# Performance work log

Hardware: AMD Instinct MI355X
Metric: run time of the kernel (lower is better)

Reference implementation:

```python
import jax, jax.numpy as jnp
import numpy as np

B = 512; LH = 200; N = 40000; F = 256; E = 2000000; EF = 4
K = 8; LP = 50; P = 5000; D = 64; TD = 16; SK = 1000


def _time_enc(t):
    # TimeDualDecayEncoder stand-in: fixed log-spaced frequency cosine features (TGAT-style)
    freqs = 1.0 / (10.0 ** (jnp.arange(TD, dtype=jnp.float32) / TD * 5.0))
    return jnp.cos(t[..., None] * freqs)


def _layernorm(x, g, b):
    m = x.mean(-1, keepdims=True)
    v = ((x - m) ** 2).mean(-1, keepdims=True)
    return (x - m) * jax.lax.rsqrt(v + 1e-5) * g + b


def _gru(x, Wih, Whh, bih, bhh):
    # torch nn.GRU (batch_first), gate order r,z,n; returns final hidden state
    bsz, H = x.shape[0], Whh.shape[1]
    def step(h, xt):
        gi = xt @ Wih.T + bih
        gh = h @ Whh.T + bhh
        ir, iz, inn = jnp.split(gi, 3, -1)
        hr, hz, hn = jnp.split(gh, 3, -1)
        r = jax.nn.sigmoid(ir + hr)
        z = jax.nn.sigmoid(iz + hz)
        n = jnp.tanh(inn + r * hn)
        return (1.0 - z) * n + z * h, None
    h, _ = jax.lax.scan(step, jnp.zeros((bsz, H), x.dtype), jnp.swapaxes(x, 0, 1))
    return h


def _forward(src_node_ids, dst_node_ids, local_neighbor_ids, local_edge_ids, local_times,
             dst_neighbor_ids, dst_edge_ids, dst_times, retrieved_indices,
             node_raw, edge_raw, pool_nodes,
             Wfeat, bfeat, Wedge, bedge, Wtime, btime, Wstruct, bstruct, ln_g, ln_b,
             gruL_Wih, gruL_Whh, gruL_bih, gruL_bhh, gruQ_Wih, gruQ_Whh, gruQ_bih, gruQ_bhh,
             gcn_W, gcn_b, fus_W, fus_b, out_W, out_b):

    def dygkt(nids, eids, times, cur_dst, cur_skill):
        raw = node_raw[nids]                                   # (B,L,F) gather
        nf = raw @ Wfeat.T + bfeat
        ef = edge_raw[eids, 0:1] @ Wedge.T + bedge
        tf = _time_enc(times) @ Wtime.T + btime
        co = (nids == cur_dst[:, None]).astype(jnp.float32)[..., None]
        st = co @ Wstruct.T + bstruct
        sim = (raw[..., 0].astype(jnp.int32) == cur_skill[:, None]).astype(jnp.float32)[..., None]
        sk = sim @ Wstruct.T + bstruct
        return _layernorm(nf + ef + tf + st + sk, ln_g, ln_b)

    def graph_emb(demo):
        # demo: (K,LP) padded node-id sequences (0 = pad). Build dedup'd undirected
        # consecutive-pair graph, run GCNConv (self loops, sym norm), mean-pool.
        ids = demo.reshape(-1)
        M = ids.shape[0]
        valid = ids > 0
        sids = jnp.sort(jnp.where(valid, ids, N))               # invalid -> sentinel N
        uniq = (sids < N) & jnp.concatenate([jnp.ones((1,), bool), sids[1:] != sids[:-1]])
        x = node_raw[jnp.clip(sids, 0, N - 1)] @ Wfeat.T + bfeat
        h = (x @ gcn_W.T) * uniq[:, None]
        u = demo[:, :-1].reshape(-1)
        v = demo[:, 1:].reshape(-1)
        ve = (u > 0) & (v > 0)
        a = jnp.minimum(u, v); b = jnp.maximum(u, v)
        BIG = N * N                                             # fits int32 since N=40000
        skey = jnp.sort(jnp.where(ve, a * N + b, BIG))
        ew = ((skey < BIG) & jnp.concatenate([jnp.ones((1,), bool), skey[1:] != skey[:-1]])).astype(x.dtype)
        su = jnp.clip(jnp.searchsorted(sids, skey // N), 0, M - 1)
        sv = jnp.clip(jnp.searchsorted(sids, skey % N), 0, M - 1)
        uf = uniq.astype(x.dtype)
        deg = jnp.zeros(M, x.dtype).at[su].add(ew).at[sv].add(ew) + uf   # + self loop
        dis = jnp.where(deg > 0, jax.lax.rsqrt(deg), 0.0)
        nrm = (ew * dis[su] * dis[sv])[:, None]
        agg = jnp.zeros_like(h).at[sv].add(nrm * h[su]).at[su].add(nrm * h[sv])
        agg = agg + h * (dis * dis)[:, None] + gcn_b * uf[:, None]
        out = jax.nn.relu(agg)
        return out.sum(0) / jnp.maximum(uniq.sum(), 1).astype(x.dtype)

    dst_skill = node_raw[dst_node_ids, 0].astype(jnp.int32)
    src_skill = node_raw[src_node_ids, 0].astype(jnp.int32)
    local_emb = _gru(dygkt(local_neighbor_ids, local_edge_ids, local_times, dst_node_ids, dst_skill),
                     gruL_Wih, gruL_Whh, gruL_bih, gruL_bhh)
    glob = jax.vmap(graph_emb)(pool_nodes[retrieved_indices])   # (B,D)
    q_emb = _gru(dygkt(dst_neighbor_ids, dst_edge_ids, dst_times, src_node_ids, src_skill),
                 gruQ_Wih, gruQ_Whh, gruQ_bih, gruQ_bhh)
    fused = jax.nn.relu(jnp.concatenate([local_emb, glob], 1) @ fus_W.T + fus_b)
    return fused @ out_W.T + out_b, q_emb @ out_W.T + out_b


def setup_inputs() -> dict:
    key = jax.random.key(0)
    ks = jax.random.split(key, 32)
    f32 = jnp.float32
    node_raw = jax.random.normal(ks[0], (N, F), f32)
    node_raw = node_raw.at[:, 0].set(jax.random.randint(ks[1], (N,), 0, SK).astype(f32))
    edge_raw = jax.random.normal(ks[2], (E, EF), f32)
    ids = jax.random.randint(ks[3], (P, LP), 1, N)
    lens = jax.random.randint(ks[4], (P,), 2, LP + 1)
    pool_nodes = jnp.where(jnp.arange(LP)[None, :] < lens[:, None], ids, 0).astype(jnp.int32)
    def lin(k, o, i, s=0.05):
        kw, kb = jax.random.split(k)
        return jax.random.normal(kw, (o, i), f32) * s, jax.random.normal(kb, (o,), f32) * s
    Wfeat, bfeat = lin(ks[5], D, F)
    Wedge, bedge = lin(ks[6], D, 1)
    Wtime, btime = lin(ks[7], D, TD)
    Wstruct, bstruct = lin(ks[8], D, 1)
    gruL_Wih, gruL_bih = lin(ks[9], 3 * D, D)
    gruL_Whh, gruL_bhh = lin(ks[10], 3 * D, D)
    gruQ_Wih, gruQ_bih = lin(ks[11], 3 * D, D)
    gruQ_Whh, gruQ_bhh = lin(ks[12], 3 * D, D)
    gcn_W, gcn_b = lin(ks[13], D, D)
    fus_W, fus_b = lin(ks[14], D, 2 * D)
    out_W, out_b = lin(ks[15], D, D)
    return dict(
        src_node_ids=jax.random.randint(ks[16], (B,), 0, N).astype(jnp.int32),
        dst_node_ids=jax.random.randint(ks[17], (B,), 0, N).astype(jnp.int32),
        local_neighbor_ids=jax.random.randint(ks[18], (B, LH), 0, N).astype(jnp.int32),
        local_edge_ids=jax.random.randint(ks[19], (B, LH), 0, E).astype(jnp.int32),
        local_times=jax.random.uniform(ks[20], (B, LH), f32) * 100.0,
        dst_neighbor_ids=jax.random.randint(ks[21], (B, LH), 0, N).astype(jnp.int32),
        dst_edge_ids=jax.random.randint(ks[22], (B, LH), 0, E).astype(jnp.int32),
        dst_times=jax.random.uniform(ks[23], (B, LH), f32) * 100.0,
        retrieved_indices=jax.random.randint(ks[24], (B, K), 0, P).astype(jnp.int32),
        node_raw=node_raw, edge_raw=edge_raw, pool_nodes=pool_nodes,
        Wfeat=Wfeat, bfeat=bfeat, Wedge=Wedge, bedge=bedge, Wtime=Wtime, btime=btime,
        Wstruct=Wstruct, bstruct=bstruct, ln_g=jnp.ones((D,), f32), ln_b=jnp.zeros((D,), f32),
        gruL_Wih=gruL_Wih, gruL_Whh=gruL_Whh, gruL_bih=gruL_bih, gruL_bhh=gruL_bhh,
        gruQ_Wih=gruQ_Wih, gruQ_Whh=gruQ_Whh, gruQ_bih=gruQ_bih, gruQ_bhh=gruQ_bhh,
        gcn_W=gcn_W, gcn_b=gcn_b, fus_W=fus_W, fus_b=fus_b, out_W=out_W, out_b=out_b)


def reference(src_node_ids, dst_node_ids, local_neighbor_ids, local_edge_ids, local_times,
              dst_neighbor_ids, dst_edge_ids, dst_times, retrieved_indices,
              node_raw, edge_raw, pool_nodes,
              Wfeat, bfeat, Wedge, bedge, Wtime, btime, Wstruct, bstruct, ln_g, ln_b,
              gruL_Wih, gruL_Whh, gruL_bih, gruL_bhh, gruQ_Wih, gruQ_Whh, gruQ_bih, gruQ_bhh,
              gcn_W, gcn_b, fus_W, fus_b, out_W, out_b):
    return _forward(src_node_ids, dst_node_ids, local_neighbor_ids, local_edge_ids, local_times,
                    dst_neighbor_ids, dst_edge_ids, dst_times, retrieved_indices,
                    node_raw, edge_raw, pool_nodes,
                    Wfeat, bfeat, Wedge, bedge, Wtime, btime, Wstruct, bstruct, ln_g, ln_b,
                    gruL_Wih, gruL_Whh, gruL_bih, gruL_bhh, gruQ_Wih, gruQ_Whh, gruQ_bih, gruQ_bhh,
                    gcn_W, gcn_b, fus_W, fus_b, out_W, out_b)
```

## Files before the change

kernel.cpp:

```cpp
#include <hip/hip_runtime.h>
#include <math.h>

#define NN 40000
#define FF 256
#define DD 64
#define LHH 200
#define BB 512
#define TDD 16
#define EE 2000000
#define GE_HASH 1024

typedef _Float16 h2f __attribute__((ext_vector_type(2)));

__constant__ float TFREQ[16] = {
    1.0f,            0.48696753f,    0.23713737f,    0.115478195f,
    0.056234132f,    0.027384196f,   0.013335215f,   0.0064938162f,
    0.0031622776f,   0.0015399265f,  0.00074989421f, 0.00036517414f,
    0.00017782794f,  8.6596433e-05f, 4.2169650e-05f, 2.0535251e-05f
};

__device__ __forceinline__ float fd2(unsigned a, unsigned b, float c) {
    union { unsigned u; h2f h; } ua, ub;
    ua.u = a; ub.u = b;
    return __builtin_amdgcn_fdot2(ua.h, ub.h, c, false);
}
__device__ __forceinline__ unsigned packrn(float a, float b) {
    union { h2f h; unsigned u; } x;
    x.h.x = (_Float16)a; x.h.y = (_Float16)b;
    return x.u;
}
__device__ __forceinline__ unsigned short f16u(float a) {
    union { _Float16 h; unsigned short u; } x;
    x.h = (_Float16)a;
    return x.u;
}
__device__ __forceinline__ float h16f(unsigned short u) {
    union { unsigned short u; _Float16 h; } x;
    x.u = u;
    return (float)x.h;
}
__device__ __forceinline__ float f16lo(unsigned u) {
    union { unsigned u; h2f h; } x; x.u = u; return (float)x.h.x;
}
__device__ __forceinline__ float f16hi(unsigned u) {
    union { unsigned u; h2f h; } x; x.u = u; return (float)x.h.y;
}
__device__ __forceinline__ unsigned pkrtz_u(float a, float b) {
    auto pk = __builtin_amdgcn_cvt_pkrtz(a, b);
    union { decltype(pk) h; unsigned u; } x;
    x.h = pk;
    return x.u;
}
__device__ __forceinline__ float dpp_xor1(float v) {
    return __int_as_float(
        __builtin_amdgcn_mov_dpp(__float_as_int(v), 0xB1, 0xF, 0xF, true));
}
__device__ __forceinline__ unsigned rlu(unsigned v, int l) {
    return (unsigned)__builtin_amdgcn_readlane((int)v, l);
}
__device__ __forceinline__ float sigm(float x) {
    return __builtin_amdgcn_rcpf(1.f + __expf(-x));
}
__device__ __forceinline__ float tanh_f(float x) {
    float e = __expf(2.f * x);
    return 1.f - 2.f * __builtin_amdgcn_rcpf(e + 1.f);
}
__device__ __forceinline__ int hlookupf(const unsigned* hkey, const int* hslot, unsigned id)
{
    unsigned p = (id * 2654435761u) & (GE_HASH - 1);
    while (hkey[p] != id) p = (p + 1) & (GE_HASH - 1);
    return hslot[p];
}

__global__ void __launch_bounds__(256)
compact_kernel(const float* __restrict__ node_raw, const float* __restrict__ edge_raw,
               unsigned short* __restrict__ skill16, unsigned short* __restrict__ e016)
{
    const int stride = gridDim.x * 256;
    int i = blockIdx.x * 256 + threadIdx.x;
    for (int n = i; n < NN; n += stride)
        skill16[n] = (unsigned short)(int)node_raw[(size_t)n * FF];
    for (int e = i; e < EE; e += stride)
        e016[e] = f16u(edge_raw[(size_t)e * 4]);
}

template<int KDIM>
__global__ void __launch_bounds__(256)
gemm_nt_kernel(const float* __restrict__ A, const float* __restrict__ W,
               const float* __restrict__ bias, float* __restrict__ C, int Nrows)
{
    __shared__ __align__(16) float a_t[128][8];
    __shared__ __align__(16) float wt[8][64];
    const int tid = threadIdx.x;
    const int tx = tid & 15;
    const int ty = tid >> 4;
    const int n0 = blockIdx.x * 128;

    float4 acc[8];
#pragma unroll
    for (int r = 0; r < 8; ++r) acc[r] = make_float4(0.f, 0.f, 0.f, 0.f);

    for (int kc = 0; kc < KDIM; kc += 8) {
        __syncthreads();
        {
            int r = tid >> 1;
            int cc = (tid & 1) * 4;
            int n = n0 + r;
            float4 v = make_float4(0.f, 0.f, 0.f, 0.f);
            if (n < Nrows) v = *(const float4*)(A + (size_t)n * KDIM + kc + cc);
            *(float4*)&a_t[r][cc] = v;
        }
        {
            int m = tid >> 2;
            int f0 = (tid & 3) * 2;
            float2 v = *(const float2*)(W + (size_t)m * KDIM + kc + f0);
            wt[f0][m] = v.x; wt[f0 + 1][m] = v.y;
        }
        __syncthreads();
        float4 w4[8];
#pragma unroll
        for (int f = 0; f < 8; ++f) w4[f] = *(float4*)&wt[f][tx * 4];
#pragma unroll
        for (int rr = 0; rr < 8; ++rr) {
            int row = ty + rr * 16;
            float4 a0 = *(float4*)&a_t[row][0];
            float4 a1 = *(float4*)&a_t[row][4];
            float av[8] = {a0.x, a0.y, a0.z, a0.w, a1.x, a1.y, a1.z, a1.w};
#pragma unroll
            for (int f = 0; f < 8; ++f) {
                acc[rr].x += av[f] * w4[f].x;
                acc[rr].y += av[f] * w4[f].y;
                acc[rr].z += av[f] * w4[f].z;
                acc[rr].w += av[f] * w4[f].w;
            }
        }
    }
    float4 bv = make_float4(0.f, 0.f, 0.f, 0.f);
    if (bias) bv = *(const float4*)(bias + tx * 4);
#pragma unroll
    for (int rr = 0; rr < 8; ++rr) {
        int n = n0 + ty + rr * 16;
        if (n < Nrows) {
            float4 o = acc[rr];
            o.x += bv.x; o.y += bv.y; o.z += bv.z; o.w += bv.w;
            *(float4*)(C + (size_t)n * DD + tx * 4) = o;
        }
    }
}

__global__ void __launch_bounds__(256)
tn_gemm_kernel(const float* __restrict__ proj,
               const float* __restrict__ WihL, const float* __restrict__ WihQ,
               const float* __restrict__ ln_g,
               unsigned short* __restrict__ TnL, unsigned short* __restrict__ TnQ,
               unsigned short* __restrict__ proj16)
{
    const float* Wih = blockIdx.y ? WihQ : WihL;
    unsigned short* Tn = blockIdx.y ? TnQ : TnL;
    __shared__ float wgT[64][193];
    __shared__ __align__(16) float4 at4[64][16];
    const int tid = threadIdx.x;
    const int n0 = blockIdx.x * 64;
    for (int i = tid; i < 192 * 64; i += 256) {
        int j = i >> 6, k = i & 63;
        wgT[k][j] = Wih[i] * ln_g[k];
    }
    for (int i = tid; i < 1024; i += 256) {
        int r = i >> 4, kc = i & 15;
        at4[r][kc] = ((const float4*)(proj + (size_t)(n0 + r) * DD))[kc];
    }
    __syncthreads();
    if (blockIdx.y == 0) {
        const float* atf = (const float*)at4;
        for (int i = tid; i < 64 * 64; i += 256)
            proj16[(size_t)(n0 + (i >> 6)) * DD + (i & 63)] = f16u(atf[i]);
    }
    const int c = tid & 63, wv = tid >> 6;
    float acc0[16], acc1[16], acc2[16];
#pragma unroll
    for (int r = 0; r < 16; ++r) { acc0[r] = 0.f; acc1[r] = 0.f; acc2[r] = 0.f; }
    for (int kc = 0; kc < 16; ++kc) {
        float w0[4], w1[4], w2[4];
#pragma unroll
        for (int q = 0; q < 4; ++q) {
            w0[q] = wgT[kc * 4 + q][c];
            w1[q] = wgT[kc * 4 + q][64 + c];
            w2[q] = wgT[kc * 4 + q][128 + c];
        }
#pragma unroll
        for (int r = 0; r < 16; ++r) {
            float4 a = at4[wv * 16 + r][kc];
            acc0[r] += a.x * w0[0] + a.y * w0[1] + a.z * w0[2] + a.w * w0[3];
            acc1[r] += a.x * w1[0] + a.y * w1[1] + a.z * w1[2] + a.w * w1[3];
            acc2[r] += a.x * w2[0] + a.y * w2[1] + a.z * w2[2] + a.w * w2[3];
        }
    }
#pragma unroll
    for (int r = 0; r < 16; ++r) {
        size_t row = (size_t)(n0 + wv * 16 + r) * 192;
        Tn[row + c]       = f16u(acc0[r]);
        Tn[row + 64 + c]  = f16u(acc1[r]);
        Tn[row + 128 + c] = f16u(acc2[r]);
    }
}

__global__ void __launch_bounds__(192)
consts_kernel(const float* __restrict__ WihL, const float* __restrict__ bihL,
              const float* __restrict__ WhhL, float* __restrict__ outL,
              unsigned* __restrict__ whpL, unsigned* __restrict__ tpkL,
              const float* __restrict__ WihQ, const float* __restrict__ bihQ,
              const float* __restrict__ WhhQ, float* __restrict__ outQ,
              unsigned* __restrict__ whpQ, unsigned* __restrict__ tpkQ,
              unsigned* __restrict__ wtpk,
              const float* __restrict__ ln_g, const float* __restrict__ ln_b,
              const float* __restrict__ Wedge, const float* __restrict__ bedge,
              const float* __restrict__ Wtime, const float* __restrict__ btime,
              const float* __restrict__ Wstruct, const float* __restrict__ bstruct)
{
    const float* Wih = blockIdx.x ? WihQ : WihL;
    const float* bih = blockIdx.x ? bihQ : bihL;
    const float* Whh = blockIdx.x ? WhhQ : WhhL;
    float* out = blockIdx.x ? outQ : outL;
    unsigned* whp = blockIdx.x ? whpQ : whpL;
    unsigned* tpk = blockIdx.x ? tpkQ : tpkL;
    const int j = threadIdx.x;
    float te = 0.f, tw = 0.f, t1 = 0.f, tb0 = 0.f, cc = 0.f;
    float tt[16];
#pragma unroll
    for (int t = 0; t < 16; ++t) tt[t] = 0.f;
    for (int k = 0; k < DD; ++k) {
        float wv = Wih[j * DD + k];
        float wg = wv * ln_g[k];
        te  += wg * Wedge[k];
        tw  += wg * Wstruct[k];
        t1  += wg;
        tb0 += wg * (bedge[k] + btime[k] + 2.f * bstruct[k]);
        cc  += wv * ln_b[k];
#pragma unroll
        for (int t = 0; t < 16; ++t) tt[t] += wg * Wtime[k * TDD + t];
    }
    out[0 * 192 + j] = te;
    out[1 * 192 + j] = tw;
    out[2 * 192 + j] = t1;
    out[3 * 192 + j] = tb0;
    out[4 * 192 + j] = cc + bih[j];
    for (int t = 0; t < 16; ++t) out[(5 + t) * 192 + j] = tt[t];
    for (int q = 0; q < 8; ++q)
        tpk[j * 8 + q] = packrn(tt[2 * q], tt[2 * q + 1]);
    if (blockIdx.x == 0 && j < 64)
        for (int q = 0; q < 8; ++q)
            wtpk[j * 8 + q] = packrn(Wtime[j * TDD + 2 * q], Wtime[j * TDD + 2 * q + 1]);
    for (int k2 = 0; k2 < 32; ++k2)
        whp[j * 32 + k2] = packrn(Whh[j * DD + 2 * k2], Whh[j * DD + 2 * k2 + 1]);
}

struct PS {
    int nid, skI;
    float tn0, tn1, tn2, pv, e0, t;
};

__global__ void __launch_bounds__(256)
pre_kernel(const int* __restrict__ nidsL, const int* __restrict__ eidsL,
           const float* __restrict__ timesL, const int* __restrict__ curL,
           const int* __restrict__ nidsQ, const int* __restrict__ eidsQ,
           const float* __restrict__ timesQ, const int* __restrict__ curQ,
           const unsigned short* __restrict__ skill16, const unsigned short* __restrict__ e016,
           const unsigned short* __restrict__ proj16,
           const unsigned short* __restrict__ TnL, const unsigned short* __restrict__ TnQ,
           const float* __restrict__ cstL, const float* __restrict__ cstQ,
           const unsigned* __restrict__ tpkL, const unsigned* __restrict__ tpkQ,
           const unsigned* __restrict__ wtpk,
           const float* __restrict__ bhhL, const float* __restrict__ bhhQ,
           const float* __restrict__ Wedge, const float* __restrict__ bedge,
           const float* __restrict__ Wtime, const float* __restrict__ btime,
           const float* __restrict__ Wstruct, const float* __restrict__ bstruct,
           unsigned* __restrict__ g01out, unsigned short* __restrict__ g2out)
{
    const int tid = threadIdx.x;
    const int d = tid & 63;
    const int seg = blockIdx.x * 4 + (tid >> 6);
    const int blk = seg >> 3, qq = seg & 7;
    const int g = blk >> 9, s = blk & 511;

    const int*            nids  = g ? nidsQ : nidsL;
    const int*            eids  = g ? eidsQ : eidsL;
    const float*          times = g ? timesQ : timesL;
    const int*            curp  = g ? curQ : curL;
    const unsigned short* Tn    = g ? TnQ : TnL;
    const float*          cst   = g ? cstQ : cstL;
    const unsigned*       tpk   = g ? tpkQ : tpkL;
    const float*          bhh   = g ? bhhQ : bhhL;

    unsigned tp0[8], tp1[8], tp2[8], wtp[8];
#pragma unroll
    for (int q4 = 0; q4 < 2; ++q4) {
        uint4 a = *(const uint4*)(tpk + (size_t)(0 * 64 + d) * 8 + 4 * q4);
        tp0[4*q4] = a.x; tp0[4*q4+1] = a.y; tp0[4*q4+2] = a.z; tp0[4*q4+3] = a.w;
        uint4 b = *(const uint4*)(tpk + (size_t)(1 * 64 + d) * 8 + 4 * q4);
        tp1[4*q4] = b.x; tp1[4*q4+1] = b.y; tp1[4*q4+2] = b.z; tp1[4*q4+3] = b.w;
        uint4 c = *(const uint4*)(tpk + (size_t)(2 * 64 + d) * 8 + 4 * q4);
        tp2[4*q4] = c.x; tp2[4*q4+1] = c.y; tp2[4*q4+2] = c.z; tp2[4*q4+3] = c.w;
        uint4 e = *(const uint4*)(wtpk + (size_t)d * 8 + 4 * q4);
        wtp[4*q4] = e.x; wtp[4*q4+1] = e.y; wtp[4*q4+2] = e.z; wtp[4*q4+3] = e.w;
    }
    const float TE0 = cst[0*192 + d], TE1 = cst[0*192 + 64 + d], TE2 = cst[0*192 + 128 + d];
    const float TW0 = cst[1*192 + d], TW1 = cst[1*192 + 64 + d], TW2 = cst[1*192 + 128 + d];
    const float T10 = cst[2*192 + d], T11 = cst[2*192 + 64 + d], T12 = cst[2*192 + 128 + d];
    const float TB0 = cst[3*192 + d], TB1 = cst[3*192 + 64 + d], TB2 = cst[3*192 + 128 + d];
    const float CC0 = cst[4*192 + d] + bhh[d];
    const float CC1 = cst[4*192 + 64 + d] + bhh[64 + d];
    const float CC2 = cst[4*192 + 128 + d];
    const float we_l = Wedge[d];
    const float ws_l = Wstruct[d];
    const float b0_l = bedge[d] + btime[d] + 2.f * bstruct[d];
    const float tfl  = TFREQ[d & 15];

    const int cur = curp[s];
    const int csk = (int)skill16[cur];
    const int* nrow = nids + s * LHH;
    const int* erow = eids + s * LHH;
    const float* trow = times + s * LHH;
    const int lbase = qq * 25;

    auto GATH = [&](PS& P, int i) {
        int l = lbase + i;
        int nid = nrow[l];
        int eid = erow[l];
        P.nid = nid;
        const unsigned short* tb = Tn + (size_t)nid * 192;
        P.tn0 = h16f(tb[d]);
        P.tn1 = h16f(tb[64 + d]);
        P.tn2 = h16f(tb[128 + d]);
        P.pv  = h16f(proj16[(size_t)nid * DD + d]);
        P.e0  = h16f(e016[eid]);
        P.skI = (int)skill16[nid];
        P.t   = trow[l];
    };

    auto EMIT = [&](const PS& P, int i) {
        float cv = __cosf(P.t * tfl);
        float cx = dpp_xor1(cv);
        unsigned cp = pkrtz_u(cv, cx);
        unsigned s0 = rlu(cp, 0),  s1 = rlu(cp, 2),  s2 = rlu(cp, 4),  s3 = rlu(cp, 6);
        unsigned s4 = rlu(cp, 8),  s5 = rlu(cp, 10), s6 = rlu(cp, 12), s7 = rlu(cp, 14);
        float tf = fd2(wtp[7], s7, fd2(wtp[6], s6, fd2(wtp[5], s5, fd2(wtp[4], s4, 0.f))));
        tf = fd2(wtp[3], s3, fd2(wtp[2], s2, fd2(wtp[1], s1, fd2(wtp[0], s0, tf))));
        float flg = ((P.nid == cur) ? 1.f : 0.f) + ((P.skI == csk) ? 1.f : 0.f);
        float f = P.pv + P.e0 * we_l + flg * ws_l + b0_l + tf;
        float mu = f;
#pragma unroll
        for (int off = 32; off; off >>= 1) mu += __shfl_xor(mu, off);
        mu *= (1.f / 64.f);
        float dv = f - mu, var = dv * dv;
#pragma unroll
        for (int off = 32; off; off >>= 1) var += __shfl_xor(var, off);
        float rs = rsqrtf(var * (1.f / 64.f) + 1e-5f);
        float c0 = fd2(tp0[7], s7, fd2(tp0[6], s6, fd2(tp0[5], s5, fd2(tp0[4], s4, 0.f))));
        c0 = fd2(tp0[3], s3, fd2(tp0[2], s2, fd2(tp0[1], s1, fd2(tp0[0], s0, c0))));
        float c1 = fd2(tp1[7], s7, fd2(tp1[6], s6, fd2(tp1[5], s5, fd2(tp1[4], s4, 0.f))));
        c1 = fd2(tp1[3], s3, fd2(tp1[2], s2, fd2(tp1[1], s1, fd2(tp1[0], s0, c1))));
        float c2 = fd2(tp2[7], s7, fd2(tp2[6], s6, fd2(tp2[5], s5, fd2(tp2[4], s4, 0.f))));
        c2 = fd2(tp2[3], s3, fd2(tp2[2], s2, fd2(tp2[1], s1, fd2(tp2[0], s0, c2))));
        float g0 = (c0 + P.tn0 + P.e0 * TE0 + flg * TW0 + TB0 - mu * T10) * rs + CC0;
        float g1 = (c1 + P.tn1 + P.e0 * TE1 + flg * TW1 + TB1 - mu * T11) * rs + CC1;
        float g2 = (c2 + P.tn2 + P.e0 * TE2 + flg * TW2 + TB2 - mu * T12) * rs + CC2;
        size_t pos = ((size_t)blk * LHH + (lbase + i)) * 64 + d;
        g01out[pos] = packrn(g0, g1);
        g2out[pos] = f16u(g2);
    };

    PS A, B, C;
    GATH(A, 0);
    GATH(B, 1);
    for (int i = 0; i < 25; ++i) {
        int inext = (i + 2 < 25) ? i + 2 : 24;
        GATH(C, inext);
        EMIT(A, i);
        A = B; B = C;
    }
}

__global__ void __launch_bounds__(64) __attribute__((amdgpu_waves_per_eu(1, 1)))
gru_lite_kernel(const unsigned* __restrict__ g01, const unsigned short* __restrict__ g2a,
                const unsigned* __restrict__ whpL, const unsigned* __restrict__ whpQ,
                const float* __restrict__ bhhL, const float* __restrict__ bhhQ,
                float* __restrict__ embL, float* __restrict__ embQ)
{
    const int blk = blockIdx.x;
    const int g = blk >> 9, s = blk & 511;
    const int d = threadIdx.x;

    const unsigned* whp = g ? whpQ : whpL;
    const float*    bhh = g ? bhhQ : bhhL;
    float*          emb = g ? embQ : embL;

    unsigned w0[32], w1[32], w2[32];
    {
        const unsigned* p0 = whp + (size_t)d * 32;
        const unsigned* p1 = whp + (size_t)(64 + d) * 32;
        const unsigned* p2 = whp + (size_t)(128 + d) * 32;
#pragma unroll
        for (int q4 = 0; q4 < 8; ++q4) {
            uint4 a = *(const uint4*)(p0 + 4 * q4);
            w0[4*q4] = a.x; w0[4*q4+1] = a.y; w0[4*q4+2] = a.z; w0[4*q4+3] = a.w;
            uint4 b = *(const uint4*)(p1 + 4 * q4);
            w1[4*q4] = b.x; w1[4*q4+1] = b.y; w1[4*q4+2] = b.z; w1[4*q4+3] = b.w;
            uint4 c = *(const uint4*)(p2 + 4 * q4);
            w2[4*q4] = c.x; w2[4*q4+1] = c.y; w2[4*q4+2] = c.z; w2[4*q4+3] = c.w;
        }
    }
#pragma unroll
    for (int i = 0; i < 32; ++i) {
        asm volatile("" : "+v"(w0[i]));
        asm volatile("" : "+v"(w1[i]));
        asm volatile("" : "+v"(w2[i]));
    }
    const float BH2 = bhh[128 + d];

    const unsigned* p01 = g01 + (size_t)blk * LHH * 64 + d;
    const unsigned short* p2 = g2a + (size_t)blk * LHH * 64 + d;

    float h = 0.f;

    auto COMPUTE = [&](unsigned pk01, unsigned pk2) {
        float g0 = f16lo(pk01), g1 = f16hi(pk01);
        float g2 = h16f((unsigned short)pk2);
        float hx = dpp_xor1(h);
        unsigned hpu = pkrtz_u(h, hx);
        float a0 = 0.f, a1 = 0.f, a2 = 0.f, e0 = 0.f, e1 = 0.f, e2 = 0.f;
#pragma unroll
        for (int q = 0; q < 32; q += 2) {
            unsigned sa = rlu(hpu, 2 * q);
            unsigned sb = rlu(hpu, 2 * q + 2);
            a0 = fd2(w0[q], sa, a0);
            a1 = fd2(w1[q], sa, a1);
            a2 = fd2(w2[q], sa, a2);
            e0 = fd2(w0[q+1], sb, e0);
            e1 = fd2(w1[q+1], sb, e1);
            e2 = fd2(w2[q+1], sb, e2);
        }
        float mv0 = a0 + e0, mv1 = a1 + e1, mv2 = a2 + e2;
        float r = sigm(g0 + mv0);
        float z = sigm(g1 + mv1);
        float n = tanh_f(g2 + r * (mv2 + BH2));
        h = (1.f - z) * n + z * h;
    };

    unsigned A01[4], A2[4], B01[4], B2[4];
#pragma unroll
    for (int i = 0; i < 4; ++i) {
        A01[i] = p01[(size_t)i * 64];
        A2[i]  = p2[(size_t)i * 64];
    }
    for (int l = 0; l < LHH; l += 8) {
#pragma unroll
        for (int i = 0; i < 4; ++i) {
            int ll = l + 4 + i;
            B01[i] = p01[(size_t)ll * 64];
            B2[i]  = p2[(size_t)ll * 64];
        }
#pragma unroll
        for (int i = 0; i < 4; ++i) COMPUTE(A01[i], A2[i]);
#pragma unroll
        for (int i = 0; i < 4; ++i) {
            int ll = l + 8 + i;
            if (ll > LHH - 1) ll = LHH - 1;
            A01[i] = p01[(size_t)ll * 64];
            A2[i]  = p2[(size_t)ll * 64];
        }
#pragma unroll
        for (int i = 0; i < 4; ++i) COMPUTE(B01[i], B2[i]);
    }
    emb[(size_t)s * DD + d] = h;
}

__global__ void __launch_bounds__(512)
dedup_kernel(const int* __restrict__ retrieved, const int* __restrict__ pool_nodes,
             int* __restrict__ slot_idG, float* __restrict__ disG,
             unsigned* __restrict__ startG, unsigned short* __restrict__ adjG,
             int* __restrict__ Ub)
{
    __shared__ unsigned hkey[GE_HASH];
    __shared__ int hslot[GE_HASH];
    __shared__ unsigned ekey[GE_HASH];
    __shared__ int ids[400];
    __shared__ int slot_id[400];
    __shared__ unsigned deg[400];
    __shared__ float dis[400];
    __shared__ unsigned elist[400];
    __shared__ unsigned scanA[400], scanB[400];
    __shared__ int cursor[400];
    __shared__ unsigned short adjS[800];
    __shared__ int pids[8];
    __shared__ int cntU, cntE;

    const int b = blockIdx.x;
    const int tid = threadIdx.x;

    if (tid < 8) pids[tid] = retrieved[b * 8 + tid];
    if (tid == 0) { cntU = 0; cntE = 0; }
    for (int i = tid; i < GE_HASH; i += 512) { hkey[i] = 0u; ekey[i] = 0u; }
    if (tid < 400) deg[tid] = 0u;
    __syncthreads();

    if (tid < 400) {
        int k = tid / 50, p = tid % 50;
        ids[tid] = pool_nodes[(size_t)pids[k] * 50 + p];
    }
    __syncthreads();

    if (tid < 400) {
        int idi = ids[tid];
        if (idi > 0) {
            unsigned id = (unsigned)idi;
            unsigned p = (id * 2654435761u) & (GE_HASH - 1);
            while (true) {
                unsigned old = atomicCAS(&hkey[p], 0u, id);
                if (old == 0u) {
                    int s = atomicAdd(&cntU, 1);
                    hslot[p] = s; slot_id[s] = idi;
                    break;
                }
                if (old == id) break;
                p = (p + 1) & (GE_HASH - 1);
            }
        }
    }
    __syncthreads();

    if (tid < 8 * 49) {
        int k = tid / 49, p = tid % 49;
        int u = ids[k * 50 + p], v = ids[k * 50 + p + 1];
        if (u > 0 && v > 0) {
            unsigned a = (unsigned)min(u, v), bb = (unsigned)max(u, v);
            unsigned key = a * 40000u + bb;
            unsigned p2 = (key * 2654435761u) & (GE_HASH - 1);
            while (true) {
                unsigned old = atomicCAS(&ekey[p2], 0u, key);
                if (old == 0u) {
                    int su = hlookupf(hkey, hslot, a);
                    int sv = hlookupf(hkey, hslot, bb);
                    int e = atomicAdd(&cntE, 1);
                    elist[e] = ((unsigned)su << 16) | (unsigned)sv;
                    atomicAdd(&deg[su], 1u);
                    atomicAdd(&deg[sv], 1u);
                    break;
                }
                if (old == key) break;
                p2 = (p2 + 1) & (GE_HASH - 1);
            }
        }
    }
    __syncthreads();

    const int U = cntU, EC = cntE;
    if (tid < 400) {
        dis[tid] = rsqrtf((float)deg[tid] + 1.0f);
        scanA[tid] = deg[tid];
    }
    __syncthreads();

    unsigned* src = scanA;
    unsigned* dst = scanB;
    for (int off = 1; off < 400; off <<= 1) {
        if (tid < 400)
            dst[tid] = src[tid] + ((tid >= off) ? src[tid - off] : 0u);
        __syncthreads();
        unsigned* t = src; src = dst; dst = t;
    }
    if (tid < 400) {
        unsigned st = src[tid] - deg[tid];
        cursor[tid] = (int)st;
        if (tid < U) startG[(size_t)b * 404 + tid] = st;
    }
    if (tid == 0) {
        startG[(size_t)b * 404 + U] = (U > 0) ? src[U - 1] : 0u;
        Ub[b] = U;
    }
    __syncthreads();

    if (tid < EC) {
        unsigned pk = elist[tid];
        int su = (int)(pk >> 16), sv = (int)(pk & 0xffffu);
        int pu = atomicAdd(&cursor[su], 1);
        adjS[pu] = (unsigned short)sv;
        int pv = atomicAdd(&cursor[sv], 1);
        adjS[pv] = (unsigned short)su;
    }
    __syncthreads();

    if (tid < 400) {
        slot_idG[(size_t)b * 400 + tid] = (tid < U) ? slot_id[tid] : 0;
        disG[(size_t)b * 400 + tid] = dis[tid];
    }
    for (int i = tid; i < 800; i += 512) {
        unsigned tot = (U > 0) ? src[U - 1] : 0u;
        adjG[(size_t)b * 800 + i] = (i < (int)tot) ? adjS[i] : (unsigned short)0;
    }
}

__global__ void __launch_bounds__(256)
gcn_agg_kernel(const float* __restrict__ hgcn, const float* __restrict__ gcn_b,
               const int* __restrict__ slot_idG, const float* __restrict__ disG,
               const unsigned* __restrict__ startG, const unsigned short* __restrict__ adjG,
               const int* __restrict__ Ub, float* __restrict__ part)
{
    __shared__ int sidS[400];
    __shared__ float disS[400];
    __shared__ unsigned stS[404];
    __shared__ unsigned short adjS[800];
    __shared__ float red[4][64];

    const int b = blockIdx.x, q = blockIdx.y;
    const int tid = threadIdx.x;
    const int lane = tid & 63, w = tid >> 6;
    const int U = Ub[b];

    for (int i = tid; i < 400; i += 256) {
        sidS[i] = slot_idG[(size_t)b * 400 + i];
        disS[i] = disG[(size_t)b * 400 + i];
    }
    for (int i = tid; i < 404; i += 256) stS[i] = startG[(size_t)b * 404 + i];
    for (int i = tid; i < 800; i += 256) adjS[i] = adjG[(size_t)b * 800 + i];
    __syncthreads();

    const float gb = gcn_b[lane];
    float acc = 0.f;

    for (int s = q * 4 + w; s < U; s += 16) {
        int nid = sidS[s];
        float ds = disS[s];
        float v = fmaf(ds * ds, hgcn[(size_t)nid * 64 + lane], gb);
        int a0 = (int)stS[s];
        int cnt = (int)stS[s + 1] - a0;
        for (int e0 = 0; e0 < cnt; e0 += 4) {
            float hv[4], nr[4];
#pragma unroll
            for (int j = 0; j < 4; ++j) {
                int e = e0 + j;
                int ec = (e < cnt) ? e : cnt - 1;
                int o = adjS[a0 + ec];
                nr[j] = (e < cnt) ? ds * disS[o] : 0.f;
                hv[j] = hgcn[(size_t)sidS[o] * 64 + lane];
            }
            v += nr[0] * hv[0] + nr[1] * hv[1] + nr[2] * hv[2] + nr[3] * hv[3];
        }
        acc += fmaxf(v, 0.f);
    }

    red[w][lane] = acc;
    __syncthreads();
    if (tid < 64)
        part[((size_t)b * 4 + q) * 64 + tid] =
            red[0][tid] + red[1][tid] + red[2][tid] + red[3][tid];
}

__global__ void __launch_bounds__(64)
head_kernel(const float* __restrict__ local_emb, const float* __restrict__ part,
            const int* __restrict__ Ub, const float* __restrict__ q_emb,
            const float* __restrict__ fus_W, const float* __restrict__ fus_b,
            const float* __restrict__ out_W, const float* __restrict__ out_b,
            float* __restrict__ out)
{
    __shared__ float cat[128];
    __shared__ float fus[64];
    __shared__ float qv[64];
    const int b = blockIdx.x, d = threadIdx.x;
    cat[d] = local_emb[(size_t)b * 64 + d];
    {
        const float* pb = part + (size_t)b * 4 * 64;
        float gsum = pb[d] + pb[64 + d] + pb[128 + d] + pb[192 + d];
        cat[64 + d] = gsum / (float)max(Ub[b], 1);
    }
    qv[d] = q_emb[(size_t)b * 64 + d];
    __syncthreads();
    float acc = fus_b[d];
    const float* fw = fus_W + (size_t)d * 128;
#pragma unroll 4
    for (int k = 0; k < 128; ++k) acc += cat[k] * fw[k];
    fus[d] = fmaxf(acc, 0.f);
    __syncthreads();
    float o0 = out_b[d], o1 = out_b[d];
    const float* ow = out_W + (size_t)d * 64;
#pragma unroll 4
    for (int k = 0; k < 64; ++k) { float ww = ow[k]; o0 += fus[k] * ww; o1 += qv[k] * ww; }
    out[(size_t)b * 64 + d] = o0;
    out[(size_t)BB * 64 + (size_t)b * 64 + d] = o1;
}

extern "C" void kernel_launch(void* const* d_in, const int* in_sizes, int n_in,
                              void* d_out, int out_size, void* d_ws, size_t ws_size,
                              hipStream_t stream)
{
    const int*   src_ids    = (const int*)d_in[0];
    const int*   dst_ids    = (const int*)d_in[1];
    const int*   l_nids     = (const int*)d_in[2];
    const int*   l_eids     = (const int*)d_in[3];
    const float* l_times    = (const float*)d_in[4];
    const int*   d_nids     = (const int*)d_in[5];
    const int*   d_eids     = (const int*)d_in[6];
    const float* d_times    = (const float*)d_in[7];
    const int*   retr       = (const int*)d_in[8];
    const float* node_raw   = (const float*)d_in[9];
    const float* edge_raw   = (const float*)d_in[10];
    const int*   pool_nodes = (const int*)d_in[11];
    const float* Wfeat  = (const float*)d_in[12];
    const float* bfeat  = (const float*)d_in[13];
    const float* Wedge  = (const float*)d_in[14];
    const float* bedge  = (const float*)d_in[15];
    const float* Wtime  = (const float*)d_in[16];
    const float* btime  = (const float*)d_in[17];
    const float* Wstruct= (const float*)d_in[18];
    const float* bstruct= (const float*)d_in[19];
    const float* ln_g   = (const float*)d_in[20];
    const float* ln_b   = (const float*)d_in[21];
    const float* gruL_Wih = (const float*)d_in[22];
    const float* gruL_Whh = (const float*)d_in[23];
    const float* gruL_bih = (const float*)d_in[24];
    const float* gruL_bhh = (const float*)d_in[25];
    const float* gruQ_Wih = (const float*)d_in[26];
    const float* gruQ_Whh = (const float*)d_in[27];
    const float* gruQ_bih = (const float*)d_in[28];
    const float* gruQ_bhh = (const float*)d_in[29];
    const float* gcn_W  = (const float*)d_in[30];
    const float* gcn_b  = (const float*)d_in[31];
    const float* fus_W  = (const float*)d_in[32];
    const float* fus_b  = (const float*)d_in[33];
    const float* out_W  = (const float*)d_in[34];
    const float* out_b  = (const float*)d_in[35];

    char* wsb = (char*)d_ws;
    auto alloc = [&](size_t bytes) -> void* {
        void* p = (void*)wsb;
        wsb += (bytes + 255) & ~(size_t)255;
        return p;
    };
    float*          proj_node = (float*)alloc((size_t)NN * DD * 4);
    float*          hgcn      = (float*)alloc((size_t)NN * DD * 4);
    unsigned short* TnL16     = (unsigned short*)alloc((size_t)NN * 192 * 2);
    unsigned short* TnQ16     = (unsigned short*)alloc((size_t)NN * 192 * 2);
    unsigned short* proj16    = (unsigned short*)alloc((size_t)NN * DD * 2);
    unsigned short* skill16   = (unsigned short*)alloc((size_t)NN * 2);
    unsigned short* e016      = (unsigned short*)alloc((size_t)EE * 2);
    float*          cstL      = (float*)alloc(4096 * 4);
    float*          cstQ      = (float*)alloc(4096 * 4);
    unsigned*       whpL      = (unsigned*)alloc(192 * 32 * 4);
    unsigned*       whpQ      = (unsigned*)alloc(192 * 32 * 4);
    unsigned*       tpkL      = (unsigned*)alloc(192 * 8 * 4);
    unsigned*       tpkQ      = (unsigned*)alloc(192 * 8 * 4);
    unsigned*       wtpk      = (unsigned*)alloc(64 * 8 * 4);
    unsigned*       g01       = (unsigned*)alloc((size_t)2 * BB * LHH * 64 * 4);
    unsigned short* g2a       = (unsigned short*)alloc((size_t)2 * BB * LHH * 64 * 2);
    int*            slot_idG  = (int*)alloc((size_t)BB * 400 * 4);
    float*          disG      = (float*)alloc((size_t)BB * 400 * 4);
    unsigned*       startG    = (unsigned*)alloc((size_t)BB * 404 * 4);
    unsigned short* adjG      = (unsigned short*)alloc((size_t)BB * 800 * 2);
    int*            Ubuf      = (int*)alloc((size_t)BB * 4);
    float*          part      = (float*)alloc((size_t)BB * 4 * 64 * 4);
    float*          local_emb = (float*)alloc((size_t)BB * DD * 4);
    float*          q_emb     = (float*)alloc((size_t)BB * DD * 4);

    dim3 g1((NN + 127) / 128);
    gemm_nt_kernel<FF><<<g1, 256, 0, stream>>>(node_raw, Wfeat, bfeat, proj_node, NN);

    compact_kernel<<<2048, 256, 0, stream>>>(node_raw, edge_raw, skill16, e016);

    consts_kernel<<<2, 192, 0, stream>>>(gruL_Wih, gruL_bih, gruL_Whh, cstL, whpL, tpkL,
                                         gruQ_Wih, gruQ_bih, gruQ_Whh, cstQ, whpQ, tpkQ,
                                         wtpk, ln_g, ln_b, Wedge, bedge, Wtime, btime,
                                         Wstruct, bstruct);

    tn_gemm_kernel<<<dim3(NN / 64, 2), 256, 0, stream>>>(proj_node, gruL_Wih, gruQ_Wih,
                                                         ln_g, TnL16, TnQ16, proj16);

    dedup_kernel<<<BB, 512, 0, stream>>>(retr, pool_nodes, slot_idG, disG,
                                         startG, adjG, Ubuf);

    pre_kernel<<<2 * BB * 2, 256, 0, stream>>>(
        l_nids, l_eids, l_times, dst_ids,
        d_nids, d_eids, d_times, src_ids,
        skill16, e016, proj16, TnL16, TnQ16, cstL, cstQ,
        tpkL, tpkQ, wtpk, gruL_bhh, gruQ_bhh,
        Wedge, bedge, Wtime, btime, Wstruct, bstruct,
        g01, g2a);

    gemm_nt_kernel<DD><<<g1, 256, 0, stream>>>(proj_node, gcn_W, nullptr, hgcn, NN);

    gru_lite_kernel<<<2 * BB, 64, 0, stream>>>(
        g01, g2a, whpL, whpQ, gruL_bhh, gruQ_bhh, local_emb, q_emb);

    gcn_agg_kernel<<<dim3(BB, 4), 256, 0, stream>>>(
        hgcn, gcn_b, slot_idG, disG, startG, adjG, Ubuf, part);

    head_kernel<<<BB, 64, 0, stream>>>(local_emb, part, Ubuf, q_emb,
        fus_W, fus_b, out_W, out_b, (float*)d_out);
}
```

Baseline: 302.9 us.

## Fuse GRU and GCN aggregation into one tail kernel; drop edge compaction pass

Removes the compact pass that converted all 2M edge features to fp16; pre_kernel now reads edge_raw directly for only the gathered edges. Merges gru_lite and gcn_agg into a single tail kernel where the first blocks run GRU recurrences (4 sequences per 256-thread block) and the rest do GCN aggregation, so the latency-bound GRU overlaps the aggregation work. The hgcn GEMM is moved earlier in the launch order. This trades lower GRU occupancy and a branchy kernel for fewer launches and much less edge-compaction traffic.

```diff
diff --git a/kernel.cpp b/kernel.cpp
--- a/kernel.cpp
+++ b/kernel.cpp
@@ -73,15 +73,10 @@
 }
 
 __global__ void __launch_bounds__(256)
-compact_kernel(const float* __restrict__ node_raw, const float* __restrict__ edge_raw,
-               unsigned short* __restrict__ skill16, unsigned short* __restrict__ e016)
-{
-    const int stride = gridDim.x * 256;
+compact_kernel(const float* __restrict__ node_raw, unsigned short* __restrict__ skill16)
+{
     int i = blockIdx.x * 256 + threadIdx.x;
-    for (int n = i; n < NN; n += stride)
-        skill16[n] = (unsigned short)(int)node_raw[(size_t)n * FF];
-    for (int e = i; e < EE; e += stride)
-        e016[e] = f16u(edge_raw[(size_t)e * 4]);
+    if (i < NN) skill16[i] = (unsigned short)(int)node_raw[(size_t)i * FF];
 }
 
 template<int KDIM>
@@ -264,7 +259,7 @@
            const float* __restrict__ timesL, const int* __restrict__ curL,
            const int* __restrict__ nidsQ, const int* __restrict__ eidsQ,
            const float* __restrict__ timesQ, const int* __restrict__ curQ,
-           const unsigned short* __restrict__ skill16, const unsigned short* __restrict__ e016,
+           const unsigned short* __restrict__ skill16, const float* __restrict__ edge_raw,
            const unsigned short* __restrict__ proj16,
            const unsigned short* __restrict__ TnL, const unsigned short* __restrict__ TnQ,
            const float* __restrict__ cstL, const float* __restrict__ cstQ,
@@ -332,7 +327,7 @@
         P.tn1 = h16f(tb[64 + d]);
         P.tn2 = h16f(tb[128 + d]);
         P.pv  = h16f(proj16[(size_t)nid * DD + d]);
-        P.e0  = h16f(e016[eid]);
+        P.e0  = edge_raw[(size_t)eid * 4];
         P.skI = (int)skill16[nid];
         P.t   = trow[l];
     };
@@ -378,100 +373,6 @@
         EMIT(A, i);
         A = B; B = C;
     }
-}
-
-__global__ void __launch_bounds__(64) __attribute__((amdgpu_waves_per_eu(1, 1)))
-gru_lite_kernel(const unsigned* __restrict__ g01, const unsigned short* __restrict__ g2a,
-                const unsigned* __restrict__ whpL, const unsigned* __restrict__ whpQ,
-                const float* __restrict__ bhhL, const float* __restrict__ bhhQ,
-                float* __restrict__ embL, float* __restrict__ embQ)
-{
-    const int blk = blockIdx.x;
-    const int g = blk >> 9, s = blk & 511;
-    const int d = threadIdx.x;
-
-    const unsigned* whp = g ? whpQ : whpL;
-    const float*    bhh = g ? bhhQ : bhhL;
-    float*          emb = g ? embQ : embL;
-
-    unsigned w0[32], w1[32], w2[32];
-    {
-        const unsigned* p0 = whp + (size_t)d * 32;
-        const unsigned* p1 = whp + (size_t)(64 + d) * 32;
-        const unsigned* p2 = whp + (size_t)(128 + d) * 32;
-#pragma unroll
-        for (int q4 = 0; q4 < 8; ++q4) {
-            uint4 a = *(const uint4*)(p0 + 4 * q4);
-            w0[4*q4] = a.x; w0[4*q4+1] = a.y; w0[4*q4+2] = a.z; w0[4*q4+3] = a.w;
-            uint4 b = *(const uint4*)(p1 + 4 * q4);
-            w1[4*q4] = b.x; w1[4*q4+1] = b.y; w1[4*q4+2] = b.z; w1[4*q4+3] = b.w;
-            uint4 c = *(const uint4*)(p2 + 4 * q4);
-            w2[4*q4] = c.x; w2[4*q4+1] = c.y; w2[4*q4+2] = c.z; w2[4*q4+3] = c.w;
-        }
-    }
-#pragma unroll
-    for (int i = 0; i < 32; ++i) {
-        asm volatile("" : "+v"(w0[i]));
-        asm volatile("" : "+v"(w1[i]));
-        asm volatile("" : "+v"(w2[i]));
-    }
-    const float BH2 = bhh[128 + d];
-
-    const unsigned* p01 = g01 + (size_t)blk * LHH * 64 + d;
-    const unsigned short* p2 = g2a + (size_t)blk * LHH * 64 + d;
-
-    float h = 0.f;
-
-    auto COMPUTE = [&](unsigned pk01, unsigned pk2) {
-        float g0 = f16lo(pk01), g1 = f16hi(pk01);
-        float g2 = h16f((unsigned short)pk2);
-        float hx = dpp_xor1(h);
-        unsigned hpu = pkrtz_u(h, hx);
-        float a0 = 0.f, a1 = 0.f, a2 = 0.f, e0 = 0.f, e1 = 0.f, e2 = 0.f;
-#pragma unroll
-        for (int q = 0; q < 32; q += 2) {
-            unsigned sa = rlu(hpu, 2 * q);
-            unsigned sb = rlu(hpu, 2 * q + 2);
-            a0 = fd2(w0[q], sa, a0);
-            a1 = fd2(w1[q], sa, a1);
-            a2 = fd2(w2[q], sa, a2);
-            e0 = fd2(w0[q+1], sb, e0);
-            e1 = fd2(w1[q+1], sb, e1);
-            e2 = fd2(w2[q+1], sb, e2);
-        }
-        float mv0 = a0 + e0, mv1 = a1 + e1, mv2 = a2 + e2;
-        float r = sigm(g0 + mv0);
-        float z = sigm(g1 + mv1);
-        float n = tanh_f(g2 + r * (mv2 + BH2));
-        h = (1.f - z) * n + z * h;
-    };
-
-    unsigned A01[4], A2[4], B01[4], B2[4];
-#pragma unroll
-    for (int i = 0; i < 4; ++i) {
-        A01[i] = p01[(size_t)i * 64];
-        A2[i]  = p2[(size_t)i * 64];
-    }
-    for (int l = 0; l < LHH; l += 8) {
-#pragma unroll
-        for (int i = 0; i < 4; ++i) {
-            int ll = l + 4 + i;
-            B01[i] = p01[(size_t)ll * 64];
-            B2[i]  = p2[(size_t)ll * 64];
-        }
-#pragma unroll
-        for (int i = 0; i < 4; ++i) COMPUTE(A01[i], A2[i]);
-#pragma unroll
-        for (int i = 0; i < 4; ++i) {
-            int ll = l + 8 + i;
-            if (ll > LHH - 1) ll = LHH - 1;
-            A01[i] = p01[(size_t)ll * 64];
-            A2[i]  = p2[(size_t)ll * 64];
-        }
-#pragma unroll
-        for (int i = 0; i < 4; ++i) COMPUTE(B01[i], B2[i]);
-    }
-    emb[(size_t)s * DD + d] = h;
 }
 
 __global__ void __launch_bounds__(512)
@@ -599,11 +500,17 @@
     }
 }
 
-__global__ void __launch_bounds__(256)
-gcn_agg_kernel(const float* __restrict__ hgcn, const float* __restrict__ gcn_b,
-               const int* __restrict__ slot_idG, const float* __restrict__ disG,
-               const unsigned* __restrict__ startG, const unsigned short* __restrict__ adjG,
-               const int* __restrict__ Ub, float* __restrict__ part)
+#define GRU_BLKS 256
+
+__global__ void __launch_bounds__(256) __attribute__((amdgpu_waves_per_eu(1, 2)))
+tail_kernel(const unsigned* __restrict__ g01, const unsigned short* __restrict__ g2a,
+            const unsigned* __restrict__ whpL, const unsigned* __restrict__ whpQ,
+            const float* __restrict__ bhhL, const float* __restrict__ bhhQ,
+            float* __restrict__ embL, float* __restrict__ embQ,
+            const float* __restrict__ hgcn, const float* __restrict__ gcn_b,
+            const int* __restrict__ slot_idG, const float* __restrict__ disG,
+            const unsigned* __restrict__ startG, const unsigned short* __restrict__ adjG,
+            const int* __restrict__ Ub, float* __restrict__ part)
 {
     __shared__ int sidS[400];
     __shared__ float disS[400];
@@ -611,48 +518,139 @@
     __shared__ unsigned short adjS[800];
     __shared__ float red[4][64];
 
-    const int b = blockIdx.x, q = blockIdx.y;
     const int tid = threadIdx.x;
-    const int lane = tid & 63, w = tid >> 6;
-    const int U = Ub[b];
-
-    for (int i = tid; i < 400; i += 256) {
-        sidS[i] = slot_idG[(size_t)b * 400 + i];
-        disS[i] = disG[(size_t)b * 400 + i];
-    }
-    for (int i = tid; i < 404; i += 256) stS[i] = startG[(size_t)b * 404 + i];
-    for (int i = tid; i < 800; i += 256) adjS[i] = adjG[(size_t)b * 800 + i];
-    __syncthreads();
-
-    const float gb = gcn_b[lane];
-    float acc = 0.f;
-
-    for (int s = q * 4 + w; s < U; s += 16) {
-        int nid = sidS[s];
-        float ds = disS[s];
-        float v = fmaf(ds * ds, hgcn[(size_t)nid * 64 + lane], gb);
-        int a0 = (int)stS[s];
-        int cnt = (int)stS[s + 1] - a0;
-        for (int e0 = 0; e0 < cnt; e0 += 4) {
-            float hv[4], nr[4];
-#pragma unroll
-            for (int j = 0; j < 4; ++j) {
-                int e = e0 + j;
-                int ec = (e < cnt) ? e : cnt - 1;
-                int o = adjS[a0 + ec];
-                nr[j] = (e < cnt) ? ds * disS[o] : 0.f;
-                hv[j] = hgcn[(size_t)sidS[o] * 64 + lane];
+
+    if (blockIdx.x < GRU_BLKS) {
+        const int blk = blockIdx.x * 4 + (tid >> 6);
+        const int g = blk >> 9, s = blk & 511;
+        const int d = tid & 63;
+
+        const unsigned* whp = g ? whpQ : whpL;
+        const float*    bhh = g ? bhhQ : bhhL;
+        float*          emb = g ? embQ : embL;
+
+        unsigned w0[32], w1[32], w2[32];
+        {
+            const unsigned* p0 = whp + (size_t)d * 32;
+            const unsigned* p1 = whp + (size_t)(64 + d) * 32;
+            const unsigned* p2 = whp + (size_t)(128 + d) * 32;
+#pragma unroll
+            for (int q4 = 0; q4 < 8; ++q4) {
+                uint4 a = *(const uint4*)(p0 + 4 * q4);
+                w0[4*q4] = a.x; w0[4*q4+1] = a.y; w0[4*q4+2] = a.z; w0[4*q4+3] = a.w;
+                uint4 b = *(const uint4*)(p1 + 4 * q4);
+                w1[4*q4] = b.x; w1[4*q4+1] = b.y; w1[4*q4+2] = b.z; w1[4*q4+3] = b.w;
+                uint4 c = *(const uint4*)(p2 + 4 * q4);
+                w2[4*q4] = c.x; w2[4*q4+1] = c.y; w2[4*q4+2] = c.z; w2[4*q4+3] = c.w;
             }
-            v += nr[0] * hv[0] + nr[1] * hv[1] + nr[2] * hv[2] + nr[3] * hv[3];
-        }
-        acc += fmaxf(v, 0.f);
-    }
-
-    red[w][lane] = acc;
-    __syncthreads();
-    if (tid < 64)
-        part[((size_t)b * 4 + q) * 64 + tid] =
-            red[0][tid] + red[1][tid] + red[2][tid] + red[3][tid];
+        }
+#pragma unroll
+        for (int i = 0; i < 32; ++i) {
+            asm volatile("" : "+v"(w0[i]));
+            asm volatile("" : "+v"(w1[i]));
+            asm volatile("" : "+v"(w2[i]));
+        }
+        const float BH2 = bhh[128 + d];
+
+        const unsigned* p01 = g01 + (size_t)blk * LHH * 64 + d;
+        const unsigned short* p2 = g2a + (size_t)blk * LHH * 64 + d;
+
+        float h = 0.f;
+
+        auto COMPUTE = [&](unsigned pk01, unsigned pk2) {
+            float g0 = f16lo(pk01), g1 = f16hi(pk01);
+            float g2 = h16f((unsigned short)pk2);
+            float hx = dpp_xor1(h);
+            unsigned hpu = pkrtz_u(h, hx);
+            float a0 = 0.f, a1 = 0.f, a2 = 0.f, e0 = 0.f, e1 = 0.f, e2 = 0.f;
+#pragma unroll
+            for (int q = 0; q < 32; q += 2) {
+                unsigned sa = rlu(hpu, 2 * q);
+                unsigned sb = rlu(hpu, 2 * q + 2);
+                a0 = fd2(w0[q], sa, a0);
+                a1 = fd2(w1[q], sa, a1);
+                a2 = fd2(w2[q], sa, a2);
+                e0 = fd2(w0[q+1], sb, e0);
+                e1 = fd2(w1[q+1], sb, e1);
+                e2 = fd2(w2[q+1], sb, e2);
+            }
+            float mv0 = a0 + e0, mv1 = a1 + e1, mv2 = a2 + e2;
+            float r = sigm(g0 + mv0);
+            float z = sigm(g1 + mv1);
+            float n = tanh_f(g2 + r * (mv2 + BH2));
+            h = (1.f - z) * n + z * h;
+        };
+
+        unsigned A01[4], A2[4], B01[4], B2[4];
+#pragma unroll
+        for (int i = 0; i < 4; ++i) {
+            A01[i] = p01[(size_t)i * 64];
+            A2[i]  = p2[(size_t)i * 64];
+        }
+        for (int l = 0; l < LHH; l += 8) {
+#pragma unroll
+            for (int i = 0; i < 4; ++i) {
+                int ll = l + 4 + i;
+                B01[i] = p01[(size_t)ll * 64];
+                B2[i]  = p2[(size_t)ll * 64];
+            }
+#pragma unroll
+            for (int i = 0; i < 4; ++i) COMPUTE(A01[i], A2[i]);
+#pragma unroll
+            for (int i = 0; i < 4; ++i) {
+                int ll = l + 8 + i;
+                if (ll > LHH - 1) ll = LHH - 1;
+                A01[i] = p01[(size_t)ll * 64];
+                A2[i]  = p2[(size_t)ll * 64];
+            }
+#pragma unroll
+            for (int i = 0; i < 4; ++i) COMPUTE(B01[i], B2[i]);
+        }
+        emb[(size_t)s * DD + d] = h;
+    } else {
+        const int blk2 = blockIdx.x - GRU_BLKS;
+        const int b = blk2 >> 2, q = blk2 & 3;
+        const int lane = tid & 63, w = tid >> 6;
+        const int U = Ub[b];
+
+        for (int i = tid; i < 400; i += 256) {
+            sidS[i] = slot_idG[(size_t)b * 400 + i];
+            disS[i] = disG[(size_t)b * 400 + i];
+        }
+        for (int i = tid; i < 404; i += 256) stS[i] = startG[(size_t)b * 404 + i];
+        for (int i = tid; i < 800; i += 256) adjS[i] = adjG[(size_t)b * 800 + i];
+        __syncthreads();
+
+        const float gb = gcn_b[lane];
+        float acc = 0.f;
+
+        for (int s = q * 4 + w; s < U; s += 16) {
+            int nid = sidS[s];
+            float ds = disS[s];
+            float v = fmaf(ds * ds, hgcn[(size_t)nid * 64 + lane], gb);
+            int a0 = (int)stS[s];
+            int cnt = (int)stS[s + 1] - a0;
+            for (int e0 = 0; e0 < cnt; e0 += 4) {
+                float hv[4], nr[4];
+#pragma unroll
+                for (int j = 0; j < 4; ++j) {
+                    int e = e0 + j;
+                    int ec = (e < cnt) ? e : cnt - 1;
+                    int o = adjS[a0 + ec];
+                    nr[j] = (e < cnt) ? ds * disS[o] : 0.f;
+                    hv[j] = hgcn[(size_t)sidS[o] * 64 + lane];
+                }
+                v += nr[0] * hv[0] + nr[1] * hv[1] + nr[2] * hv[2] + nr[3] * hv[3];
+            }
+            acc += fmaxf(v, 0.f);
+        }
+
+        red[w][lane] = acc;
+        __syncthreads();
+        if (tid < 64)
+            part[((size_t)b * 4 + q) * 64 + tid] =
+                red[0][tid] + red[1][tid] + red[2][tid] + red[3][tid];
+    }
 }
 
 __global__ void __launch_bounds__(64)
@@ -741,7 +739,6 @@
     unsigned short* TnQ16     = (unsigned short*)alloc((size_t)NN * 192 * 2);
     unsigned short* proj16    = (unsigned short*)alloc((size_t)NN * DD * 2);
     unsigned short* skill16   = (unsigned short*)alloc((size_t)NN * 2);
-    unsigned short* e016      = (unsigned short*)alloc((size_t)EE * 2);
     float*          cstL      = (float*)alloc(4096 * 4);
     float*          cstQ      = (float*)alloc(4096 * 4);
     unsigned*       whpL      = (unsigned*)alloc(192 * 32 * 4);
@@ -763,13 +760,15 @@
     dim3 g1((NN + 127) / 128);
     gemm_nt_kernel<FF><<<g1, 256, 0, stream>>>(node_raw, Wfeat, bfeat, proj_node, NN);
 
-    compact_kernel<<<2048, 256, 0, stream>>>(node_raw, edge_raw, skill16, e016);
+    compact_kernel<<<(NN + 255) / 256, 256, 0, stream>>>(node_raw, skill16);
 
     consts_kernel<<<2, 192, 0, stream>>>(gruL_Wih, gruL_bih, gruL_Whh, cstL, whpL, tpkL,
                                          gruQ_Wih, gruQ_bih, gruQ_Whh, cstQ, whpQ, tpkQ,
                                          wtpk, ln_g, ln_b, Wedge, bedge, Wtime, btime,
                                          Wstruct, bstruct);
 
+    gemm_nt_kernel<DD><<<g1, 256, 0, stream>>>(proj_node, gcn_W, nullptr, hgcn, NN);
+
     tn_gemm_kernel<<<dim3(NN / 64, 2), 256, 0, stream>>>(proj_node, gruL_Wih, gruQ_Wih,
                                                          ln_g, TnL16, TnQ16, proj16);
 
@@ -779,17 +778,13 @@
     pre_kernel<<<2 * BB * 2, 256, 0, stream>>>(
         l_nids, l_eids, l_times, dst_ids,
         d_nids, d_eids, d_times, src_ids,
-        skill16, e016, proj16, TnL16, TnQ16, cstL, cstQ,
+        skill16, edge_raw, proj16, TnL16, TnQ16, cstL, cstQ,
         tpkL, tpkQ, wtpk, gruL_bhh, gruQ_bhh,
         Wedge, bedge, Wtime, btime, Wstruct, bstruct,
         g01, g2a);
 
-    gemm_nt_kernel<DD><<<g1, 256, 0, stream>>>(proj_node, gcn_W, nullptr, hgcn, NN);
-
-    gru_lite_kernel<<<2 * BB, 64, 0, stream>>>(
-        g01, g2a, whpL, whpQ, gruL_bhh, gruQ_bhh, local_emb, q_emb);
-
-    gcn_agg_kernel<<<dim3(BB, 4), 256, 0, stream>>>(
+    tail_kernel<<<GRU_BLKS + BB * 4, 256, 0, stream>>>(
+        g01, g2a, whpL, whpQ, gruL_bhh, gruQ_bhh, local_emb, q_emb,
         hgcn, gcn_b, slot_idG, disG, startG, adjG, Ubuf, part);
 
     head_kernel<<<BB, 64, 0, stream>>>(local_emb, part, Ubuf, q_emb,
```

After: 315.4 us. 1.04x slower.
